# Kernel tuning notes

Hardware: AMD Instinct MI355X
Metric: run time of the kernel (lower is better)

Reference implementation:

```python
import jax, jax.numpy as jnp
import numpy as np

B, T, N, H, P = 16, 64, 512, 128, 12


def _laplacian_with_self_loop(adj):
    a = adj + jnp.eye(adj.shape[0], dtype=adj.dtype)
    d_inv_sqrt = 1.0 / jnp.sqrt(a.sum(axis=1))
    return a * d_inv_sqrt[:, None] * d_inv_sqrt[None, :]


def setup_inputs() -> dict:
    key = jax.random.key(0)
    ks = jax.random.split(key, 10)
    inputs = jax.random.normal(ks[0], (B, T, N), dtype=jnp.float32)
    adj = jax.random.uniform(ks[1], (N, N), dtype=jnp.float32)
    adj = (adj + adj.T) * 0.5
    laplacian = _laplacian_with_self_loop(adj)

    def xavier(k, shape):
        fan_in, fan_out = shape[0], shape[1]
        lim = np.sqrt(6.0 / (fan_in + fan_out))
        return jax.random.uniform(k, shape, jnp.float32, -lim, lim)

    W1 = xavier(ks[2], (H + 1, 2 * H))      # graph_conv1 weights
    b1 = jnp.ones((2 * H,), jnp.float32)    # bias init 1.0
    W2 = xavier(ks[3], (H + 1, H))          # graph_conv2 weights
    b2 = jnp.zeros((H,), jnp.float32)
    att_w1 = xavier(ks[4], (H, 1))
    att_w2 = xavier(ks[5], (N, 1))
    att_w3 = xavier(ks[6], (N, 1))
    att_b1 = jnp.zeros((1,), jnp.float32)
    att_b2 = jnp.zeros((1,), jnp.float32)
    att_b3 = jnp.zeros((1,), jnp.float32)
    W_out = xavier(ks[7], (T, P))
    b_out = jnp.zeros((P,), jnp.float32)
    return dict(inputs=inputs, laplacian=laplacian, W1=W1, b1=b1, W2=W2, b2=b2,
                att_w1=att_w1, att_w2=att_w2, att_w3=att_w3,
                att_b1=att_b1, att_b2=att_b2, att_b3=att_b3,
                W_out=W_out, b_out=b_out)


def reference(inputs, laplacian, W1, b1, W2, b2,
              att_w1, att_w2, att_w3, att_b1, att_b2, att_b3,
              W_out, b_out):
    Bs, Ts, Ns = inputs.shape
    Hs = W2.shape[1]

    def graph_conv(x_t, h_flat, W, b):
        # x_t: [B,N]; h_flat: [B, N*H]
        h = h_flat.reshape(Bs, Ns, Hs)
        conc = jnp.concatenate([x_t[..., None], h], axis=-1)     # [B,N,H+1]
        agg = jnp.einsum('mn,bnc->bmc', laplacian, conc)          # [B,N,H+1]
        out = agg @ W + b                                         # [B,N,O]
        return out.reshape(Bs, -1)                                # [B,N*O] (flattened, matching torch)

    def step(h_flat, x_t):
        ru = jax.nn.sigmoid(graph_conv(x_t, h_flat, W1, b1))      # [B, N*2H]
        r, u = jnp.split(ru, 2, axis=1)                            # split on flattened dim (faithful)
        c = jnp.tanh(graph_conv(x_t, r * h_flat, W2, b2))          # [B, N*H]
        new_h = u * h_flat + (1.0 - u) * c
        return new_h, new_h

    h0 = jnp.zeros((Bs, Ns * Hs), inputs.dtype)
    _, hs = jax.lax.scan(step, h0, jnp.moveaxis(inputs, 1, 0))     # [T,B,N*H]
    hidden_states = jnp.moveaxis(hs, 0, 1).reshape(Bs, Ts, Ns, Hs)

    # SelfAttention: project H->1, then N->1 per (b,t), softmax over T
    hs1 = hidden_states.reshape(-1, Hs) @ att_w1 + att_b1          # [B*T*N, 1]
    f = (hs1.reshape(-1, Ns) @ att_w2 + att_b2).reshape(Bs, Ts)
    g = (hs1.reshape(-1, Ns) @ att_w3 + att_b3).reshape(Bs, Ts)
    beta = jax.nn.softmax(g * f, axis=-1)                          # [B,T]
    context = beta[:, :, None] * hs1.reshape(Bs, Ts, Ns)           # [B,T,N]

    context = context.transpose(0, 2, 1)                           # [B,N,T]
    Ps = W_out.shape[1]
    out = (context.reshape(-1, Ts) @ W_out + b_out).reshape(Bs, Ns, Ps)
    return out.transpose(0, 2, 1)                                  # [B,pre_len,N]
```

## Files before the change

kernel.cpp:

```cpp
#include <hip/hip_runtime.h>
#include <math.h>

#define B_ 16
#define T_ 64
#define N_ 512
#define H_ 128
#define P_ 12
#define NH 65536

__global__ __launch_bounds__(512) void lx_kernel(const float* __restrict__ x,
                                                 const float* __restrict__ L,
                                                 float* __restrict__ Lx) {
    __shared__ __align__(16) float xs[2][N_];
    const int r0 = blockIdx.x * 2;
    const int tid = threadIdx.x;
    for (int j = 0; j < 2; ++j)
        xs[j][tid] = x[(size_t)(r0 + j) * N_ + tid];
    __syncthreads();
    float a0 = 0.f, a1 = 0.f;
    const int m = tid;
#pragma unroll 8
    for (int n = 0; n < N_; ++n) {
        float lv = L[(size_t)n * N_ + m];
        a0 += xs[0][n] * lv;
        a1 += xs[1][n] * lv;
    }
    Lx[(size_t)(r0 + 0) * N_ + m] = a0;
    Lx[(size_t)(r0 + 1) * N_ + m] = a1;
}

#define FMA4(dst, a, hv)                                                      \
    dst[0] += (a) * (hv).x; dst[1] += (a) * (hv).y;                           \
    dst[2] += (a) * (hv).z; dst[3] += (a) * (hv).w;

__global__ __launch_bounds__(512) void gc1y_kernel(
    const float* __restrict__ L, const float* __restrict__ Hprev,
    const float* __restrict__ Lx, const float* __restrict__ W1,
    const float* __restrict__ b1, const float* __restrict__ W2,
    float* __restrict__ Y, float* __restrict__ u, int t) {
    __shared__ __align__(16) union Buf {
        float Ht[2][32][H_];
        struct { float R[32][H_]; float Zb[16][H_]; } s;
    } bb;
    __shared__ __align__(16) union LW {
        float Lt[2][32][20];
        float Wt[16][260];
    } sm;

    const int tid = threadIdx.x;
    const int b = blockIdx.x & 15;
    const int m0 = (blockIdx.x >> 4) * 16;
    const float* __restrict__ Hb = Hprev + (size_t)b * NH;

    const int hrow = tid >> 5, hcol = (tid & 31) * 4;
    const int lm = tid >> 5, lk = tid & 31;

    {
        *(float4*)&bb.Ht[0][hrow][hcol] =
            *(const float4*)&Hb[(size_t)hrow * H_ + hcol];
        *(float4*)&bb.Ht[0][hrow + 16][hcol] =
            *(const float4*)&Hb[(size_t)(hrow + 16) * H_ + hcol];
        sm.Lt[0][lk][lm] = L[(size_t)(m0 + lm) * N_ + lk];
    }
    __syncthreads();

    const int g = tid >> 6;
    const int l = tid & 63;
    const int ty = l >> 4;
    const int tx = l & 15;
    const int ma0 = ty * 4;
    const int ca0 = tx * 4, cb0 = 64 + tx * 4;

    float acc[4][2][4] = {};

    for (int kc = 0; kc < 16; ++kc) {
        const int bi = kc & 1, bj = bi ^ 1;
        float4 p0, p1;
        float pl;
        if (kc < 15) {
            const size_t kb = (size_t)(kc + 1) * 32;
            p0 = *(const float4*)&Hb[(kb + hrow) * H_ + hcol];
            p1 = *(const float4*)&Hb[(kb + hrow + 16) * H_ + hcol];
            pl = L[(size_t)(m0 + lm) * N_ + kb + lk];
        }
#pragma unroll
        for (int kk = 0; kk < 4; ++kk) {
            const int k = g * 4 + kk;
            const float4 la = *(const float4*)&sm.Lt[bi][k][ma0];
            const float4 h0 = *(const float4*)&bb.Ht[bi][k][ca0];
            const float4 h1 = *(const float4*)&bb.Ht[bi][k][cb0];
            FMA4(acc[0][0], la.x, h0) FMA4(acc[0][1], la.x, h1)
            FMA4(acc[1][0], la.y, h0) FMA4(acc[1][1], la.y, h1)
            FMA4(acc[2][0], la.z, h0) FMA4(acc[2][1], la.z, h1)
            FMA4(acc[3][0], la.w, h0) FMA4(acc[3][1], la.w, h1)
        }
        if (kc < 15) {
            *(float4*)&bb.Ht[bj][hrow][hcol] = p0;
            *(float4*)&bb.Ht[bj][hrow + 16][hcol] = p1;
            sm.Lt[bj][lk][lm] = pl;
        }
        __syncthreads();
    }

    for (int r = 0; r < 8; ++r) {
        if (g == r) {
#pragma unroll
            for (int i = 0; i < 4; ++i) {
#pragma unroll
                for (int v = 0; v < 2; ++v) {
                    const int c = v ? cb0 : ca0;
                    float4* zp = (float4*)&bb.s.Zb[ma0 + i][c];
                    if (r == 0) {
                        *zp = make_float4(acc[i][v][0], acc[i][v][1],
                                          acc[i][v][2], acc[i][v][3]);
                    } else {
                        float4 z = *zp;
                        *zp = make_float4(z.x + acc[i][v][0], z.y + acc[i][v][1],
                                          z.z + acc[i][v][2], z.w + acc[i][v][3]);
                    }
                }
            }
        }
        __syncthreads();
    }

    const int to = tid & 63, tm = tid >> 6;
    const int o0 = to * 4;
    float a2[2][4] = {};
    const int wr = tid >> 5, wc = (tid & 31) * 4;

    for (int ck = 0; ck < 8; ++ck) {
        *(float4*)&sm.Wt[wr][wc] =
            *(const float4*)&W1[(size_t)(1 + ck * 16 + wr) * 256 + wc];
        *(float4*)&sm.Wt[wr][wc + 128] =
            *(const float4*)&W1[(size_t)(1 + ck * 16 + wr) * 256 + wc + 128];
        __syncthreads();
#pragma unroll
        for (int ch4 = 0; ch4 < 4; ++ch4) {
            const float4 w0v = *(const float4*)&sm.Wt[ch4 * 4 + 0][o0];
            const float4 w1v = *(const float4*)&sm.Wt[ch4 * 4 + 1][o0];
            const float4 w2v = *(const float4*)&sm.Wt[ch4 * 4 + 2][o0];
            const float4 w3v = *(const float4*)&sm.Wt[ch4 * 4 + 3][o0];
            const int cc = ck * 16 + ch4 * 4;
#pragma unroll
            for (int i = 0; i < 2; ++i) {
                const float4 zv = *(const float4*)&bb.s.Zb[tm + 8 * i][cc];
                a2[i][0] += zv.x * w0v.x + zv.y * w1v.x + zv.z * w2v.x + zv.w * w3v.x;
                a2[i][1] += zv.x * w0v.y + zv.y * w1v.y + zv.z * w2v.y + zv.w * w3v.y;
                a2[i][2] += zv.x * w0v.z + zv.y * w1v.z + zv.z * w2v.z + zv.w * w3v.z;
                a2[i][3] += zv.x * w0v.w + zv.y * w1v.w + zv.z * w2v.w + zv.w * w3v.w;
            }
        }
        __syncthreads();
    }

    const float4 w0r = *(const float4*)&W1[o0];
    const float4 bbv = *(const float4*)&b1[o0];
    const float* __restrict__ LxRow = Lx + ((size_t)b * T_ + t) * N_ + m0;
    const bool isR = (m0 < 256);

    if (isR) {
#pragma unroll
        for (int i = 0; i < 2; ++i) {
            const int mi = tm + 8 * i;
            const float lx = LxRow[mi];
            float v0 = a2[i][0] + lx * w0r.x + bbv.x;
            float v1 = a2[i][1] + lx * w0r.y + bbv.y;
            float v2 = a2[i][2] + lx * w0r.z + bbv.z;
            float v3 = a2[i][3] + lx * w0r.w + bbv.w;
            float s0 = 1.f / (1.f + expf(-v0));
            float s1 = 1.f / (1.f + expf(-v1));
            float s2 = 1.f / (1.f + expf(-v2));
            float s3 = 1.f / (1.f + expf(-v3));
            const int fl = (m0 + mi) * 256 + o0;
            float4 hv = *(const float4*)&Hb[fl];
            const int rr2 = 2 * mi + (o0 >> 7);
            *(float4*)&bb.s.R[rr2][o0 & 127] =
                make_float4(s0 * hv.x, s1 * hv.y, s2 * hv.z, s3 * hv.w);
        }
        __syncthreads();

        const int rr = tid >> 5;
        const int oc = (tid & 31) * 4;
        float a3[2][4] = {};
        for (int ck = 0; ck < 8; ++ck) {
            *(float4*)&sm.Wt[wr][wc] =
                *(const float4*)&W2[(size_t)(1 + ck * 16 + wr) * H_ + wc];
            __syncthreads();
#pragma unroll
            for (int ch4 = 0; ch4 < 4; ++ch4) {
                const float4 w0v = *(const float4*)&sm.Wt[ch4 * 4 + 0][oc];
                const float4 w1v = *(const float4*)&sm.Wt[ch4 * 4 + 1][oc];
                const float4 w2v = *(const float4*)&sm.Wt[ch4 * 4 + 2][oc];
                const float4 w3v = *(const float4*)&sm.Wt[ch4 * 4 + 3][oc];
                const int cc = ck * 16 + ch4 * 4;
#pragma unroll
                for (int i = 0; i < 2; ++i) {
                    const float4 zv = *(const float4*)&bb.s.R[rr + 16 * i][cc];
                    a3[i][0] += zv.x * w0v.x + zv.y * w1v.x + zv.z * w2v.x + zv.w * w3v.x;
                    a3[i][1] += zv.x * w0v.y + zv.y * w1v.y + zv.z * w2v.y + zv.w * w3v.y;
                    a3[i][2] += zv.x * w0v.z + zv.y * w1v.z + zv.z * w2v.z + zv.w * w3v.z;
                    a3[i][3] += zv.x * w0v.w + zv.y * w1v.w + zv.z * w2v.w + zv.w * w3v.w;
                }
            }
            __syncthreads();
        }
        float* __restrict__ Yb = Y + (size_t)b * NH;
#pragma unroll
        for (int i = 0; i < 2; ++i) {
            *(float4*)&Yb[(size_t)(2 * m0 + rr + 16 * i) * H_ + oc] =
                make_float4(a3[i][0], a3[i][1], a3[i][2], a3[i][3]);
        }
    } else {
        float* __restrict__ uB = u + (size_t)b * NH;
#pragma unroll
        for (int i = 0; i < 2; ++i) {
            const int mi = tm + 8 * i;
            const float lx = LxRow[mi];
            float v0 = a2[i][0] + lx * w0r.x + bbv.x;
            float v1 = a2[i][1] + lx * w0r.y + bbv.y;
            float v2 = a2[i][2] + lx * w0r.z + bbv.z;
            float v3 = a2[i][3] + lx * w0r.w + bbv.w;
            float s0 = 1.f / (1.f + expf(-v0));
            float s1 = 1.f / (1.f + expf(-v1));
            float s2 = 1.f / (1.f + expf(-v2));
            float s3 = 1.f / (1.f + expf(-v3));
            const int fl = (m0 + mi) * 256 + o0;
            *(float4*)&uB[fl - NH] = make_float4(s0, s1, s2, s3);
        }
    }
}

__global__ __launch_bounds__(512) void gcz_kernel(
    const float* __restrict__ L, const float* __restrict__ Y,
    const float* __restrict__ Hprev, const float* __restrict__ u,
    const float* __restrict__ Lx, const float* __restrict__ W2,
    const float* __restrict__ b2, const float* __restrict__ aw1,
    const float* __restrict__ ab1, float* __restrict__ Hnew,
    float* __restrict__ hs1, int t) {
    __shared__ __align__(16) union Buf {
        float Ht[2][32][H_];
        struct { float R[32][H_]; float Zb[16][H_]; } s;
    } bb;
    __shared__ __align__(16) float Lt[2][32][20];

    const int tid = threadIdx.x;
    const int b = blockIdx.x & 15;
    const int m0 = (blockIdx.x >> 4) * 16;
    const float* __restrict__ Yb = Y + (size_t)b * NH;

    const int hrow = tid >> 5, hcol = (tid & 31) * 4;
    const int lm = tid >> 5, lk = tid & 31;

    {
        *(float4*)&bb.Ht[0][hrow][hcol] =
            *(const float4*)&Yb[(size_t)hrow * H_ + hcol];
        *(float4*)&bb.Ht[0][hrow + 16][hcol] =
            *(const float4*)&Yb[(size_t)(hrow + 16) * H_ + hcol];
        Lt[0][lk][lm] = L[(size_t)(m0 + lm) * N_ + lk];
    }
    __syncthreads();

    const int g = tid >> 6;
    const int l = tid & 63;
    const int ty = l >> 4;
    const int tx = l & 15;
    const int ma0 = ty * 4;
    const int ca0 = tx * 4, cb0 = 64 + tx * 4;

    float acc[4][2][4] = {};

    for (int kc = 0; kc < 16; ++kc) {
        const int bi = kc & 1, bj = bi ^ 1;
        float4 p0, p1;
        float pl;
        if (kc < 15) {
            const size_t kb = (size_t)(kc + 1) * 32;
            p0 = *(const float4*)&Yb[(kb + hrow) * H_ + hcol];
            p1 = *(const float4*)&Yb[(kb + hrow + 16) * H_ + hcol];
            pl = L[(size_t)(m0 + lm) * N_ + kb + lk];
        }
#pragma unroll
        for (int kk = 0; kk < 4; ++kk) {
            const int k = g * 4 + kk;
            const float4 la = *(const float4*)&Lt[bi][k][ma0];
            const float4 h0 = *(const float4*)&bb.Ht[bi][k][ca0];
            const float4 h1 = *(const float4*)&bb.Ht[bi][k][cb0];
            FMA4(acc[0][0], la.x, h0) FMA4(acc[0][1], la.x, h1)
            FMA4(acc[1][0], la.y, h0) FMA4(acc[1][1], la.y, h1)
            FMA4(acc[2][0], la.z, h0) FMA4(acc[2][1], la.z, h1)
            FMA4(acc[3][0], la.w, h0) FMA4(acc[3][1], la.w, h1)
        }
        if (kc < 15) {
            *(float4*)&bb.Ht[bj][hrow][hcol] = p0;
            *(float4*)&bb.Ht[bj][hrow + 16][hcol] = p1;
            Lt[bj][lk][lm] = pl;
        }
        __syncthreads();
    }

    for (int r = 0; r < 8; ++r) {
        if (g == r) {
#pragma unroll
            for (int i = 0; i < 4; ++i) {
#pragma unroll
                for (int v = 0; v < 2; ++v) {
                    const int c = v ? cb0 : ca0;
                    float4* zp = (float4*)&bb.s.Zb[ma0 + i][c];
                    if (r == 0) {
                        *zp = make_float4(acc[i][v][0], acc[i][v][1],
                                          acc[i][v][2], acc[i][v][3]);
                    } else {
                        float4 z = *zp;
                        *zp = make_float4(z.x + acc[i][v][0], z.y + acc[i][v][1],
                                          z.z + acc[i][v][2], z.w + acc[i][v][3]);
                    }
                }
            }
        }
        __syncthreads();
    }

    const int zr = tid >> 5;
    const int zc = (tid & 31) * 4;
    const float4 zv = *(const float4*)&bb.s.Zb[zr][zc];
    const float4 w0r = *(const float4*)&W2[zc];
    const float4 bbv = *(const float4*)&b2[zc];
    const float4 awv = *(const float4*)&aw1[zc];
    const float lx = Lx[((size_t)b * T_ + t) * N_ + m0 + zr];

    float c0 = tanhf(zv.x + lx * w0r.x + bbv.x);
    float c1 = tanhf(zv.y + lx * w0r.y + bbv.y);
    float c2 = tanhf(zv.z + lx * w0r.z + bbv.z);
    float c3 = tanhf(zv.w + lx * w0r.w + bbv.w);

    const size_t fl = (size_t)b * NH + (size_t)(m0 + zr) * H_ + zc;
    const float4 uv = *(const float4*)&u[fl];
    const float4 hp = *(const float4*)&Hprev[fl];
    const float h0 = uv.x * hp.x + (1.f - uv.x) * c0;
    const float h1 = uv.y * hp.y + (1.f - uv.y) * c1;
    const float h2 = uv.z * hp.z + (1.f - uv.z) * c2;
    const float h3 = uv.w * hp.w + (1.f - uv.w) * c3;
    *(float4*)&Hnew[fl] = make_float4(h0, h1, h2, h3);

    float part = h0 * awv.x + h1 * awv.y + h2 * awv.z + h3 * awv.w;
#pragma unroll
    for (int off = 16; off; off >>= 1) part += __shfl_xor(part, off);
    if ((tid & 31) == 0)
        hs1[((size_t)b * T_ + t) * N_ + m0 + zr] = part + ab1[0];
}

__global__ __launch_bounds__(64) void att_beta_kernel(
    const float* __restrict__ hs1, const float* __restrict__ aw2,
    const float* __restrict__ aw3, const float* __restrict__ ab2,
    const float* __restrict__ ab3, float* __restrict__ beta) {
    const int b = blockIdx.x;
    const int t = threadIdx.x;
    const float* __restrict__ row = hs1 + ((size_t)b * T_ + t) * N_;
    float f = 0.f, g = 0.f;
    for (int n = 0; n < N_; n += 4) {
        float4 hv = *(const float4*)&row[n];
        float4 w2v = *(const float4*)&aw2[n];
        float4 w3v = *(const float4*)&aw3[n];
        f += hv.x * w2v.x + hv.y * w2v.y + hv.z * w2v.z + hv.w * w2v.w;
        g += hv.x * w3v.x + hv.y * w3v.y + hv.z * w3v.z + hv.w * w3v.w;
    }
    f += ab2[0];
    g += ab3[0];
    float s = f * g;
    float mx = s;
    for (int off = 32; off; off >>= 1) mx = fmaxf(mx, __shfl_xor(mx, off));
    float e = expf(s - mx);
    float sum = e;
    for (int off = 32; off; off >>= 1) sum += __shfl_xor(sum, off);
    beta[b * T_ + t] = e / sum;
}

__global__ __launch_bounds__(256) void att_out_kernel(
    const float* __restrict__ hs1, const float* __restrict__ beta,
    const float* __restrict__ Wout, const float* __restrict__ bout,
    float* __restrict__ out) {
    __shared__ float bs[T_];
    __shared__ float ws[T_][P_];
    const int b = blockIdx.x;
    const int tid = threadIdx.x;
    if (tid < T_) bs[tid] = beta[b * T_ + tid];
    for (int i = tid; i < T_ * P_; i += 256) ws[i / P_][i % P_] = Wout[i];
    __syncthreads();
    for (int nn = 0; nn < 2; ++nn) {
        const int n = tid + nn * 256;
        float acc[P_];
#pragma unroll
        for (int p = 0; p < P_; ++p) acc[p] = bout[p];
        for (int t = 0; t < T_; ++t) {
            float v = bs[t] * hs1[((size_t)b * T_ + t) * N_ + n];
#pragma unroll
            for (int p = 0; p < P_; ++p) acc[p] += v * ws[t][p];
        }
#pragma unroll
        for (int p = 0; p < P_; ++p) out[((size_t)b * P_ + p) * N_ + n] = acc[p];
    }
}

extern "C" void kernel_launch(void* const* d_in, const int* in_sizes, int n_in,
                              void* d_out, int out_size, void* d_ws, size_t ws_size,
                              hipStream_t stream) {
    const float* x = (const float*)d_in[0];
    const float* L = (const float*)d_in[1];
    const float* W1 = (const float*)d_in[2];
    const float* b1 = (const float*)d_in[3];
    const float* W2 = (const float*)d_in[4];
    const float* b2 = (const float*)d_in[5];
    const float* aw1 = (const float*)d_in[6];
    const float* aw2 = (const float*)d_in[7];
    const float* aw3 = (const float*)d_in[8];
    const float* ab1 = (const float*)d_in[9];
    const float* ab2 = (const float*)d_in[10];
    const float* ab3 = (const float*)d_in[11];
    const float* Wout = (const float*)d_in[12];
    const float* bout = (const float*)d_in[13];
    float* out = (float*)d_out;

    float* ws = (float*)d_ws;
    float* Lx = ws;
    float* hs1 = Lx + B_ * T_ * N_;
    float* hb0 = hs1 + B_ * T_ * N_;
    float* hb1 = hb0 + (size_t)B_ * NH;
    float* u = hb1 + (size_t)B_ * NH;
    float* Ybuf = u + (size_t)B_ * NH;
    float* beta = Ybuf + (size_t)B_ * NH;
    (void)in_sizes; (void)n_in; (void)out_size; (void)ws_size;

    hipMemsetAsync(hb0, 0, (size_t)B_ * NH * sizeof(float), stream);
    lx_kernel<<<512, 512, 0, stream>>>(x, L, Lx);

    for (int t = 0; t < T_; ++t) {
        float* hp = (t & 1) ? hb1 : hb0;
        float* hn = (t & 1) ? hb0 : hb1;
        gc1y_kernel<<<512, 512, 0, stream>>>(L, hp, Lx, W1, b1, W2, Ybuf, u, t);
        gcz_kernel<<<512, 512, 0, stream>>>(L, Ybuf, hp, u, Lx, W2, b2, aw1,
                                            ab1, hn, hs1, t);
    }
    att_beta_kernel<<<16, 64, 0, stream>>>(hs1, aw2, aw3, ab2, ab3, beta);
    att_out_kernel<<<16, 256, 0, stream>>>(hs1, beta, Wout, bout, out);
}
```

Before: 3.618 ms.

## Pair r and u rows per block in gc1y to remove r/u branch imbalance

Each block of gc1y now handles 8 rows from the first half (r part) and the matching 8 rows from the second half (u part) instead of 16 contiguous rows. Before, half the blocks ran the extra W2 projection and half did not. Now every block does the same amount of work and the divergent branch is gone. The W1 and W2 tiles are also staged 32 rows at a time, halving the number of syncs per weight pass at the cost of a larger shared weight buffer.

```diff
diff --git a/kernel.cpp b/kernel.cpp
--- a/kernel.cpp
+++ b/kernel.cpp
@@ -40,27 +40,29 @@
     float* __restrict__ Y, float* __restrict__ u, int t) {
     __shared__ __align__(16) union Buf {
         float Ht[2][32][H_];
-        struct { float R[32][H_]; float Zb[16][H_]; } s;
+        struct { float R[16][H_]; float Zb[16][H_]; } s;
     } bb;
     __shared__ __align__(16) union LW {
         float Lt[2][32][20];
-        float Wt[16][260];
+        float Wt[32][260];
     } sm;
 
     const int tid = threadIdx.x;
     const int b = blockIdx.x & 15;
-    const int m0 = (blockIdx.x >> 4) * 16;
+    const int mt = blockIdx.x >> 4;
+    const int m0 = mt * 8;
     const float* __restrict__ Hb = Hprev + (size_t)b * NH;
 
     const int hrow = tid >> 5, hcol = (tid & 31) * 4;
     const int lm = tid >> 5, lk = tid & 31;
+    const int lrow = (lm < 8) ? (m0 + lm) : (248 + m0 + lm);
 
     {
         *(float4*)&bb.Ht[0][hrow][hcol] =
             *(const float4*)&Hb[(size_t)hrow * H_ + hcol];
         *(float4*)&bb.Ht[0][hrow + 16][hcol] =
             *(const float4*)&Hb[(size_t)(hrow + 16) * H_ + hcol];
-        sm.Lt[0][lk][lm] = L[(size_t)(m0 + lm) * N_ + lk];
+        sm.Lt[0][lk][lm] = L[(size_t)lrow * N_ + lk];
     }
     __syncthreads();
 
@@ -81,7 +83,7 @@
             const size_t kb = (size_t)(kc + 1) * 32;
             p0 = *(const float4*)&Hb[(kb + hrow) * H_ + hcol];
             p1 = *(const float4*)&Hb[(kb + hrow + 16) * H_ + hcol];
-            pl = L[(size_t)(m0 + lm) * N_ + kb + lk];
+            pl = L[(size_t)lrow * N_ + kb + lk];
         }
 #pragma unroll
         for (int kk = 0; kk < 4; ++kk) {
@@ -127,21 +129,23 @@
     const int to = tid & 63, tm = tid >> 6;
     const int o0 = to * 4;
     float a2[2][4] = {};
-    const int wr = tid >> 5, wc = (tid & 31) * 4;
-
-    for (int ck = 0; ck < 8; ++ck) {
-        *(float4*)&sm.Wt[wr][wc] =
-            *(const float4*)&W1[(size_t)(1 + ck * 16 + wr) * 256 + wc];
-        *(float4*)&sm.Wt[wr][wc + 128] =
-            *(const float4*)&W1[(size_t)(1 + ck * 16 + wr) * 256 + wc + 128];
-        __syncthreads();
-#pragma unroll
-        for (int ch4 = 0; ch4 < 4; ++ch4) {
+    const int wr32 = tid >> 4;
+    const int wcb = (tid & 15) * 16;
+
+#pragma unroll 1
+    for (int ck = 0; ck < 4; ++ck) {
+#pragma unroll
+        for (int q = 0; q < 4; ++q)
+            *(float4*)&sm.Wt[wr32][wcb + 4 * q] =
+                *(const float4*)&W1[(size_t)(1 + ck * 32 + wr32) * 256 + wcb + 4 * q];
+        __syncthreads();
+#pragma unroll
+        for (int ch4 = 0; ch4 < 8; ++ch4) {
             const float4 w0v = *(const float4*)&sm.Wt[ch4 * 4 + 0][o0];
             const float4 w1v = *(const float4*)&sm.Wt[ch4 * 4 + 1][o0];
             const float4 w2v = *(const float4*)&sm.Wt[ch4 * 4 + 2][o0];
             const float4 w3v = *(const float4*)&sm.Wt[ch4 * 4 + 3][o0];
-            const int cc = ck * 16 + ch4 * 4;
+            const int cc = ck * 32 + ch4 * 4;
 #pragma unroll
             for (int i = 0; i < 2; ++i) {
                 const float4 zv = *(const float4*)&bb.s.Zb[tm + 8 * i][cc];
@@ -156,79 +160,68 @@
 
     const float4 w0r = *(const float4*)&W1[o0];
     const float4 bbv = *(const float4*)&b1[o0];
-    const float* __restrict__ LxRow = Lx + ((size_t)b * T_ + t) * N_ + m0;
-    const bool isR = (m0 < 256);
-
-    if (isR) {
-#pragma unroll
-        for (int i = 0; i < 2; ++i) {
-            const int mi = tm + 8 * i;
-            const float lx = LxRow[mi];
-            float v0 = a2[i][0] + lx * w0r.x + bbv.x;
-            float v1 = a2[i][1] + lx * w0r.y + bbv.y;
-            float v2 = a2[i][2] + lx * w0r.z + bbv.z;
-            float v3 = a2[i][3] + lx * w0r.w + bbv.w;
-            float s0 = 1.f / (1.f + expf(-v0));
-            float s1 = 1.f / (1.f + expf(-v1));
-            float s2 = 1.f / (1.f + expf(-v2));
-            float s3 = 1.f / (1.f + expf(-v3));
-            const int fl = (m0 + mi) * 256 + o0;
-            float4 hv = *(const float4*)&Hb[fl];
-            const int rr2 = 2 * mi + (o0 >> 7);
-            *(float4*)&bb.s.R[rr2][o0 & 127] =
-                make_float4(s0 * hv.x, s1 * hv.y, s2 * hv.z, s3 * hv.w);
-        }
-        __syncthreads();
-
-        const int rr = tid >> 5;
-        const int oc = (tid & 31) * 4;
-        float a3[2][4] = {};
-        for (int ck = 0; ck < 8; ++ck) {
-            *(float4*)&sm.Wt[wr][wc] =
-                *(const float4*)&W2[(size_t)(1 + ck * 16 + wr) * H_ + wc];
-            __syncthreads();
-#pragma unroll
-            for (int ch4 = 0; ch4 < 4; ++ch4) {
-                const float4 w0v = *(const float4*)&sm.Wt[ch4 * 4 + 0][oc];
-                const float4 w1v = *(const float4*)&sm.Wt[ch4 * 4 + 1][oc];
-                const float4 w2v = *(const float4*)&sm.Wt[ch4 * 4 + 2][oc];
-                const float4 w3v = *(const float4*)&sm.Wt[ch4 * 4 + 3][oc];
-                const int cc = ck * 16 + ch4 * 4;
-#pragma unroll
-                for (int i = 0; i < 2; ++i) {
-                    const float4 zv = *(const float4*)&bb.s.R[rr + 16 * i][cc];
-                    a3[i][0] += zv.x * w0v.x + zv.y * w1v.x + zv.z * w2v.x + zv.w * w3v.x;
-                    a3[i][1] += zv.x * w0v.y + zv.y * w1v.y + zv.z * w2v.y + zv.w * w3v.y;
-                    a3[i][2] += zv.x * w0v.z + zv.y * w1v.z + zv.z * w2v.z + zv.w * w3v.z;
-                    a3[i][3] += zv.x * w0v.w + zv.y * w1v.w + zv.z * w2v.w + zv.w * w3v.w;
-                }
-            }
-            __syncthreads();
-        }
-        float* __restrict__ Yb = Y + (size_t)b * NH;
-#pragma unroll
-        for (int i = 0; i < 2; ++i) {
-            *(float4*)&Yb[(size_t)(2 * m0 + rr + 16 * i) * H_ + oc] =
-                make_float4(a3[i][0], a3[i][1], a3[i][2], a3[i][3]);
-        }
-    } else {
+    const float* __restrict__ LxRow = Lx + ((size_t)b * T_ + t) * N_;
+
+    {
+        const float lx = LxRow[m0 + tm];
+        float v0 = a2[0][0] + lx * w0r.x + bbv.x;
+        float v1 = a2[0][1] + lx * w0r.y + bbv.y;
+        float v2 = a2[0][2] + lx * w0r.z + bbv.z;
+        float v3 = a2[0][3] + lx * w0r.w + bbv.w;
+        float s0 = 1.f / (1.f + expf(-v0));
+        float s1 = 1.f / (1.f + expf(-v1));
+        float s2 = 1.f / (1.f + expf(-v2));
+        float s3 = 1.f / (1.f + expf(-v3));
+        const int fl = (m0 + tm) * 256 + o0;
+        float4 hv = *(const float4*)&Hb[fl];
+        const int rr2 = 2 * tm + (o0 >> 7);
+        *(float4*)&bb.s.R[rr2][o0 & 127] =
+            make_float4(s0 * hv.x, s1 * hv.y, s2 * hv.z, s3 * hv.w);
+    }
+    {
+        const float lx = LxRow[256 + m0 + tm];
+        float v0 = a2[1][0] + lx * w0r.x + bbv.x;
+        float v1 = a2[1][1] + lx * w0r.y + bbv.y;
+        float v2 = a2[1][2] + lx * w0r.z + bbv.z;
+        float v3 = a2[1][3] + lx * w0r.w + bbv.w;
+        float s0 = 1.f / (1.f + expf(-v0));
+        float s1 = 1.f / (1.f + expf(-v1));
+        float s2 = 1.f / (1.f + expf(-v2));
+        float s3 = 1.f / (1.f + expf(-v3));
         float* __restrict__ uB = u + (size_t)b * NH;
-#pragma unroll
-        for (int i = 0; i < 2; ++i) {
-            const int mi = tm + 8 * i;
-            const float lx = LxRow[mi];
-            float v0 = a2[i][0] + lx * w0r.x + bbv.x;
-            float v1 = a2[i][1] + lx * w0r.y + bbv.y;
-            float v2 = a2[i][2] + lx * w0r.z + bbv.z;
-            float v3 = a2[i][3] + lx * w0r.w + bbv.w;
-            float s0 = 1.f / (1.f + expf(-v0));
-            float s1 = 1.f / (1.f + expf(-v1));
-            float s2 = 1.f / (1.f + expf(-v2));
-            float s3 = 1.f / (1.f + expf(-v3));
-            const int fl = (m0 + mi) * 256 + o0;
-            *(float4*)&uB[fl - NH] = make_float4(s0, s1, s2, s3);
-        }
-    }
+        *(float4*)&uB[(m0 + tm) * 256 + o0] = make_float4(s0, s1, s2, s3);
+    }
+    __syncthreads();
+
+    const int rr = tid >> 5;
+    const int oc = (tid & 31) * 4;
+    const int wc2 = (tid & 15) * 8;
+    float a3[4] = {0.f, 0.f, 0.f, 0.f};
+#pragma unroll 1
+    for (int ck = 0; ck < 4; ++ck) {
+        *(float4*)&sm.Wt[wr32][wc2] =
+            *(const float4*)&W2[(size_t)(1 + ck * 32 + wr32) * H_ + wc2];
+        *(float4*)&sm.Wt[wr32][wc2 + 4] =
+            *(const float4*)&W2[(size_t)(1 + ck * 32 + wr32) * H_ + wc2 + 4];
+        __syncthreads();
+#pragma unroll
+        for (int ch4 = 0; ch4 < 8; ++ch4) {
+            const float4 w0v = *(const float4*)&sm.Wt[ch4 * 4 + 0][oc];
+            const float4 w1v = *(const float4*)&sm.Wt[ch4 * 4 + 1][oc];
+            const float4 w2v = *(const float4*)&sm.Wt[ch4 * 4 + 2][oc];
+            const float4 w3v = *(const float4*)&sm.Wt[ch4 * 4 + 3][oc];
+            const int cc = ck * 32 + ch4 * 4;
+            const float4 zv = *(const float4*)&bb.s.R[rr][cc];
+            a3[0] += zv.x * w0v.x + zv.y * w1v.x + zv.z * w2v.x + zv.w * w3v.x;
+            a3[1] += zv.x * w0v.y + zv.y * w1v.y + zv.z * w2v.y + zv.w * w3v.y;
+            a3[2] += zv.x * w0v.z + zv.y * w1v.z + zv.z * w2v.z + zv.w * w3v.z;
+            a3[3] += zv.x * w0v.w + zv.y * w1v.w + zv.z * w2v.w + zv.w * w3v.w;
+        }
+        __syncthreads();
+    }
+    float* __restrict__ Yb = Y + (size_t)b * NH;
+    *(float4*)&Yb[(size_t)(2 * m0 + rr) * H_ + oc] =
+        make_float4(a3[0], a3[1], a3[2], a3[3]);
 }
 
 __global__ __launch_bounds__(512) void gcz_kernel(
```

Result: slower. 4.377 ms (+21.0%).
